# Optimization experiments

Hardware: AMD Instinct MI355X
Metric: run time of the kernel (lower is better)

## Reference

```python
import jax, jax.numpy as jnp
import numpy as np

N = 50000        # nodes
E = 600000       # edges (avg degree 12)
NODE, EDGE, GDIM = 15, 10, 8
HID, L, H = 128, 3, 4
D = HID // H     # per-head dim = 32


def setup_inputs() -> dict:
    key = jax.random.key(0)
    ks = jax.random.split(key, 32)
    f = lambda i, shape, s=0.05: jax.random.normal(ks[i], shape, dtype=jnp.float32) * s
    return {
        "x": f(0, (N, NODE), 1.0),
        "edge_index": jax.random.randint(ks[1], (2, E), 0, N, dtype=jnp.int32),
        "edge_attr": f(2, (E, EDGE), 1.0),
        "u": f(3, (GDIM,), 1.0),
        "enc_w": f(4, (NODE, HID)), "enc_b": f(5, (HID,)),
        "gat_lin_w": f(6, (L, HID, HID)),
        "gat_att_src": f(7, (L, H, D)), "gat_att_dst": f(8, (L, H, D)),
        "gat_lin_edge": f(9, (L, EDGE, HID)), "gat_att_edge": f(10, (L, H, D)),
        "gat_bias": f(11, (L, HID)),
        "ln_g": jnp.ones((L, HID), jnp.float32), "ln_b": jnp.zeros((L, HID), jnp.float32),
        "pool_w": f(12, (3 * HID + GDIM, GDIM)), "pool_b": f(13, (GDIM,)),
        "pool_ln_g": jnp.ones((GDIM,), jnp.float32), "pool_ln_b": jnp.zeros((GDIM,), jnp.float32),
        "head_w1": f(14, (4, HID, 32)), "head_b1": f(15, (4, 32)),
        "head_w2": f(16, (4, 32, 1)), "head_b2": f(17, (4, 1)),
        "strat_w1": f(18, (HID, 32)), "strat_b1": f(19, (32,)),
        "strat_w2": f(20, (32, 5)), "strat_b2": f(21, (5,)),
        "glob_w1": f(22, (GDIM, 32)), "glob_b1": f(23, (32,)),
        "glob_w2": f(24, (32, 4)), "glob_b2": f(25, (4,)),
    }


def _layer_norm(x, g, b, eps=1e-5):
    mu = jnp.mean(x, axis=-1, keepdims=True)
    var = jnp.mean(jnp.square(x - mu), axis=-1, keepdims=True)
    return (x - mu) * jax.lax.rsqrt(var + eps) * g + b


def _forward(edge_index, x, edge_attr, u, enc_w, enc_b, gat_lin_w, gat_att_src,
             gat_att_dst, gat_lin_edge, gat_att_edge, gat_bias, ln_g, ln_b,
             pool_w, pool_b, pool_ln_g, pool_ln_b, head_w1, head_b1, head_w2,
             head_b2, strat_w1, strat_b1, strat_w2, strat_b2, glob_w1, glob_b1,
             glob_w2, glob_b2):
    src0, dst0 = edge_index[0], edge_index[1]
    # PyG GATConv add_self_loops=True with fill_value='mean': self-loop edge
    # attr for node i = mean of edge_attr over edges whose dst is i.
    cnt = jax.ops.segment_sum(jnp.ones((E,), jnp.float32), dst0, num_segments=N)
    ea_self = jax.ops.segment_sum(edge_attr, dst0, num_segments=N) / jnp.maximum(cnt, 1.0)[:, None]
    loop = jnp.arange(N, dtype=src0.dtype)
    src = jnp.concatenate([src0, loop])
    dst = jnp.concatenate([dst0, loop])
    ea = jnp.concatenate([edge_attr, ea_self], axis=0)   # [E+N, EDGE]

    h = jax.nn.relu(x @ enc_w + enc_b)                   # node encoder [N, HID]
    for l in range(L):
        hp = (h @ gat_lin_w[l]).reshape(N, H, D)         # projected nodes
        a_s = jnp.sum(hp * gat_att_src[l], axis=-1)      # [N, H]
        a_d = jnp.sum(hp * gat_att_dst[l], axis=-1)
        ep = (ea @ gat_lin_edge[l]).reshape(-1, H, D)    # [E+N, H, D]
        a_e = jnp.sum(ep * gat_att_edge[l], axis=-1)     # [E+N, H]
        alpha = jax.nn.leaky_relu(a_s[src] + a_d[dst] + a_e, negative_slope=0.2)
        # numerically-stable softmax over incoming edges per dst node
        m = jax.ops.segment_max(alpha, dst, num_segments=N)
        w = jnp.exp(alpha - m[dst])
        denom = jax.ops.segment_sum(w, dst, num_segments=N)
        attn = w / denom[dst]                            # every node has a self-loop
        out = jax.ops.segment_sum(hp[src] * attn[..., None], dst, num_segments=N)
        out = out.reshape(N, HID) + gat_bias[l]
        # residual (shapes match) + dropout(eval=id) + layer norm
        h = _layer_norm(h + out, ln_g[l], ln_b[l])

    pooled = jnp.concatenate([h.mean(0), h.max(0), h.sum(0), u])[None]  # [1, 3*HID+GDIM]
    g = _layer_norm(jax.nn.relu(pooled @ pool_w + pool_b), pool_ln_g, pool_ln_b)

    # four stacked 128->32->1 heads (priority:tanh, coop/urgency/safety:sigmoid)
    z = jax.nn.relu(jnp.einsum('nf,kfh->knh', h, head_w1) + head_b1[:, None, :])
    y = jnp.einsum('knh,kho->kno', z, head_w2) + head_b2[:, None, :]   # [4, N, 1]
    priority = jnp.tanh(y[0])
    cooperation = jax.nn.sigmoid(y[1])
    urgency = jax.nn.sigmoid(y[2])
    safety = jax.nn.sigmoid(y[3])
    strategies = jax.nn.softmax(jax.nn.relu(h @ strat_w1 + strat_b1) @ strat_w2 + strat_b2, axis=-1)
    global_signal = jnp.tanh(jax.nn.relu(g @ glob_w1 + glob_b1) @ glob_w2 + glob_b2)[0]  # [4]
    return (priority, cooperation, urgency, safety, strategies, global_signal)


def reference(x, edge_index, edge_attr, u, enc_w, enc_b, gat_lin_w, gat_att_src,
              gat_att_dst, gat_lin_edge, gat_att_edge, gat_bias, ln_g, ln_b,
              pool_w, pool_b, pool_ln_g, pool_ln_b, head_w1, head_b1, head_w2,
              head_b2, strat_w1, strat_b1, strat_w2, strat_b2, glob_w1, glob_b1,
              glob_w2, glob_b2):
    return _forward(edge_index, x, edge_attr, u, enc_w, enc_b, gat_lin_w,
                    gat_att_src, gat_att_dst, gat_lin_edge, gat_att_edge,
                    gat_bias, ln_g, ln_b, pool_w, pool_b, pool_ln_g, pool_ln_b,
                    head_w1, head_b1, head_w2, head_b2, strat_w1, strat_b1,
                    strat_w2, strat_b2, glob_w1, glob_b1, glob_w2, glob_b2)
```

## Files before the change

### kernel.cpp

```cpp
#include <hip/hip_runtime.h>
#include <hip/hip_bf16.h>
#include <hip/hip_fp16.h>

#define N_NODES 50000
#define N_EDGES 600000
#define TOT_E   (N_EDGES + N_NODES)
#define NLAYER  3
#define PB      200
#define SCB     512
#define NSB     ((N_NODES + SCB - 1)/SCB)
#define CAP     96

typedef __hip_bfloat16 bf16;
typedef __attribute__((ext_vector_type(8))) short short8;
typedef __attribute__((ext_vector_type(4))) float floatx4;

__device__ __forceinline__ float b2f(bf16 v){ return __bfloat162float(v); }

__device__ __forceinline__ float ldm(const void* p, long i, int m){
  return m ? ((const float*)p)[i] : b2f(((const bf16*)p)[i]);
}

__device__ __forceinline__ unsigned bfr(float f){
  unsigned u = __float_as_uint(f);
  return (u + 0x7fffu + ((u>>16)&1u)) >> 16;
}

__global__ void detect_kernel(const void* probe, int* mode){
  __shared__ float red[256];
  int t = threadIdx.x;
  const bf16* p = (const bf16*)probe;
  float mx = 0.f;
  for (int i = t; i < 1920; i += 256){
    float v = fabsf(b2f(p[i]));
    if (!isfinite(v)) v = 1e30f;
    mx = fmaxf(mx, v);
  }
  red[t] = mx; __syncthreads();
  if (t == 0){
    float m = 0.f;
    for (int i = 0; i < 256; i++) m = fmaxf(m, red[i]);
    mode[0] = (m > 1000.0f) ? 1 : 0;
  }
}

__global__ void sentinel_kernel(int host_code, const int* devflags, const int* mode, float* out){
  if (threadIdx.x == 0 && blockIdx.x == 0){
    int code = host_code;
    if (!code && devflags){
      if (devflags[1] > 900)      code = 16384;
      else if (devflags[0])       code = 20480;
    }
    if (code){
      if (mode) code += 512*mode[0];
      out[0] = (float)code;
    }
  }
}

struct CvtTab { const void* s[27]; float* d[27]; int n[27]; };
__global__ void cvt_small_kernel(CvtTab tab, const int* mode){
  int b = blockIdx.x;
  int i = blockIdx.y*256 + threadIdx.x;
  if (i < tab.n[b]) tab.d[b][i] = ldm(tab.s[b], i, mode[0]);
}

__global__ void count_kernel(const int* __restrict__ ei, int* __restrict__ cnt, int* devflags){
  int e = blockIdx.x*256 + threadIdx.x;
  if (e >= N_EDGES) return;
  int s = ei[e], d = ei[N_EDGES + e];
  if (((unsigned)s >= N_NODES) || ((unsigned)d >= N_NODES)) atomicOr(&devflags[0], 1);
  else atomicAdd(&cnt[d], 1);
  if (e < 1024 && ei[2*e + 1] == 0) atomicAdd(&devflags[1], 1);
}

__global__ __launch_bounds__(SCB) void scan1_kernel(const int* __restrict__ cnt, int* __restrict__ bsum){
  __shared__ int ws[SCB/64];
  int i = blockIdx.x*SCB + threadIdx.x;
  int v = (i < N_NODES) ? cnt[i] + 1 : 0;
  int lane = threadIdx.x & 63, w = threadIdx.x >> 6;
  #pragma unroll
  for (int off = 1; off < 64; off <<= 1) v += __shfl_xor(v, off);
  if (lane == 0) ws[w] = v;
  __syncthreads();
  if (threadIdx.x == 0){
    int s = 0;
    #pragma unroll
    for (int k = 0; k < SCB/64; k++) s += ws[k];
    bsum[blockIdx.x] = s;
  }
}

__global__ void scan2_kernel(int* __restrict__ bsum, int* __restrict__ rowptr){
  if (threadIdx.x == 0 && blockIdx.x == 0){
    int run = 0;
    for (int b = 0; b < NSB; b++){ int t = bsum[b]; bsum[b] = run; run += t; }
    rowptr[N_NODES] = run;
  }
}

__global__ __launch_bounds__(SCB) void scan3_kernel(const int* __restrict__ cnt, const int* __restrict__ bsum,
                                                    int* __restrict__ rowptr){
  __shared__ int sm[SCB];
  int t = threadIdx.x;
  int i = blockIdx.x*SCB + t;
  int v = (i < N_NODES) ? cnt[i] + 1 : 0;
  sm[t] = v; __syncthreads();
  for (int off = 1; off < SCB; off <<= 1){
    int add = (t >= off) ? sm[t-off] : 0;
    __syncthreads();
    sm[t] += add;
    __syncthreads();
  }
  if (i < N_NODES) rowptr[i] = bsum[blockIdx.x] + sm[t] - v;
}

__global__ void scatter_kernel(const int* __restrict__ ei, const int* __restrict__ rowptr,
                               int* __restrict__ fill, int* __restrict__ srcs, int* __restrict__ pos_of){
  int e = blockIdx.x*256 + threadIdx.x;
  if (e >= TOT_E) return;
  if (e < N_EDGES){
    int s = ei[e], d = ei[N_EDGES + e];
    int pos = rowptr[d] + atomicAdd(&fill[d], 1);
    srcs[pos] = s; pos_of[e] = pos;
  } else {
    int i = e - N_EDGES;
    srcs[rowptr[i+1] - 1] = i;
  }
}

__global__ void pack_kernel(const float* __restrict__ head_w1, const float* __restrict__ strat_w1,
                            const float* __restrict__ head_b1, const float* __restrict__ strat_b1,
                            float* __restrict__ W1cat, float* __restrict__ b1cat){
  int t = blockIdx.x*256 + threadIdx.x;
  if (t < 128*160){
    int f = t / 160, c = t % 160;
    W1cat[t] = (c < 128) ? head_w1[(c>>5)*4096 + f*32 + (c&31)]
                         : strat_w1[f*32 + (c-128)];
  }
  if (t < 160) b1cat[t] = (t < 128) ? head_b1[t] : strat_b1[t-128];
}

__global__ void mmat_kernel(const float* __restrict__ We, const float* __restrict__ att_edge,
                            float* __restrict__ M){
  int t = threadIdx.x;
  if (t >= 120) return;
  int l = t / 40, r = t % 40, k = r / 4, hh = r % 4;
  float s = 0;
  #pragma unroll
  for (int d = 0; d < 32; d++)
    s += We[l*1280 + k*128 + hh*32 + d] * att_edge[l*128 + hh*32 + d];
  M[t] = s;
}

__global__ void vsd_kernel(const float* __restrict__ Wl, const float* __restrict__ att_src,
                           const float* __restrict__ att_dst, float* __restrict__ vsd){
  int t = blockIdx.x*256 + threadIdx.x;
  if (t >= 3*128*8) return;
  int l = t >> 10, r = t & 1023;
  int k = r >> 3, c = r & 7;
  int sd = c >> 2, hh = c & 3;
  const float* w = Wl + l*16384 + k*128 + hh*32;
  const float* a = (sd ? att_dst : att_src) + l*128 + hh*32;
  float s = 0;
  #pragma unroll
  for (int d = 0; d < 32; d++) s += w[d]*a[d];
  vsd[t] = s;
}

__global__ void pack_bsw_kernel(const float* __restrict__ Wl, const float* __restrict__ vsd,
                                const float* __restrict__ W1cat,
                                ushort* __restrict__ Bsw0, ushort* __restrict__ Bsw1){
  int tid = blockIdx.x*256 + threadIdx.x;
  if (tid < 3*4*144*32){
    int l = tid / 18432, rr = tid % 18432;
    int kt = rr / 4608, r2 = rr % 4608;
    int n = r2 / 32, kk = r2 & 31;
    int k = kt*32 + kk;
    float f;
    if (n < 128)      f = Wl[l*16384 + k*128 + n];
    else if (n < 136) f = vsd[l*1024 + k*8 + (n - 128)];
    else              f = 0.f;
    unsigned hb = bfr(f);
    float fh = __uint_as_float(hb<<16);
    unsigned lb = bfr(f - fh);
    Bsw0[(size_t)(l*2+0)*18432 + kt*4608 + n*32 + kk] = (ushort)hb;
    Bsw0[(size_t)(l*2+1)*18432 + kt*4608 + n*32 + kk] = (ushort)lb;
  } else {
    int t2 = tid - 3*4*144*32;
    if (t2 >= 4*160*32) return;
    int kt = t2 / 5120, r2 = t2 % 5120;
    int n = r2 / 32, kk = r2 & 31;
    int k = kt*32 + kk;
    float f = W1cat[k*160 + n];
    unsigned hb = bfr(f);
    float fh = __uint_as_float(hb<<16);
    unsigned lb = bfr(f - fh);
    Bsw1[kt*5120 + n*32 + kk]          = (ushort)hb;
    Bsw1[4*5120 + kt*5120 + n*32 + kk] = (ushort)lb;
  }
}

__global__ __launch_bounds__(128) void encoder_kernel(const void* __restrict__ x_raw, const int* __restrict__ mode,
                                                      const float* __restrict__ enc_w, const float* __restrict__ enc_b,
                                                      float* __restrict__ h){
  __shared__ float xs[16];
  int n = blockIdx.x, j = threadIdx.x;
  if (j < 15) xs[j] = ldm(x_raw, (long)n*15 + j, mode[0]);
  __syncthreads();
  float acc = enc_b[j];
  #pragma unroll
  for (int k = 0; k < 15; k++) acc += xs[k] * enc_w[k*128 + j];
  h[(size_t)n*128 + j] = fmaxf(acc, 0.0f);
}

__global__ void ae_kernel(const void* __restrict__ ea_raw, const int* __restrict__ mode,
                          const float* __restrict__ Mmat, const int* __restrict__ pos_of,
                          float4* __restrict__ aec){
  int e = blockIdx.x*256 + threadIdx.x;
  if (e >= N_EDGES) return;
  int m = mode[0];
  float v[10];
  #pragma unroll
  for (int k = 0; k < 10; k++) v[k] = ldm(ea_raw, (long)e*10 + k, m);
  int p = pos_of[e];
  #pragma unroll
  for (int l = 0; l < 3; l++){
    float r[4];
    #pragma unroll
    for (int hh = 0; hh < 4; hh++){
      float s = 0;
      #pragma unroll
      for (int k = 0; k < 10; k++) s += v[k]*Mmat[l*40 + k*4 + hh];
      r[hh] = s;
    }
    aec[(size_t)l*TOT_E + p] = make_float4(r[0], r[1], r[2], r[3]);
  }
}

template<int NT, int MODE>
__global__ __launch_bounds__(256) void gemm_mfma(
    const float* __restrict__ A, const ushort* __restrict__ Bhi, const ushort* __restrict__ Blo,
    int M, const float* __restrict__ bias, __half* __restrict__ Ch, float* __restrict__ Cf,
    float* __restrict__ a_s, float* __restrict__ a_d){
  int wv = threadIdx.x >> 6, lane = threadIdx.x & 63;
  int nl = lane & 15, q = lane >> 4;
  int row0 = blockIdx.x*64 + wv*16;
  if (row0 >= M) return;
  floatx4 acc[NT];
  #pragma unroll
  for (int t = 0; t < NT; t++) acc[t] = (floatx4){0.f, 0.f, 0.f, 0.f};
  int ra = row0 + nl; if (ra > M-1) ra = M-1;
  const float* arow = A + (size_t)ra*128 + q*8;
  #pragma unroll
  for (int kt = 0; kt < 4; kt++){
    float4 a0 = *(const float4*)(arow + kt*32);
    float4 a1 = *(const float4*)(arow + kt*32 + 4);
    float af[8] = {a0.x,a0.y,a0.z,a0.w,a1.x,a1.y,a1.z,a1.w};
    short8 ahi, alo;
    #pragma unroll
    for (int j = 0; j < 8; j++){
      unsigned hb = bfr(af[j]);
      float fh = __uint_as_float(hb<<16);
      unsigned lb = bfr(af[j] - fh);
      ahi[j] = (short)hb; alo[j] = (short)lb;
    }
    const ushort* bh = Bhi + kt*(NT*16*32) + nl*32 + q*8;
    const ushort* bl = Blo + kt*(NT*16*32) + nl*32 + q*8;
    #pragma unroll
    for (int t = 0; t < NT; t++){
      short8 b0 = *(const short8*)(bh + t*512);
      short8 b1 = *(const short8*)(bl + t*512);
      acc[t] = __builtin_amdgcn_mfma_f32_16x16x32_bf16(ahi, b0, acc[t], 0, 0, 0);
      acc[t] = __builtin_amdgcn_mfma_f32_16x16x32_bf16(alo, b0, acc[t], 0, 0, 0);
      acc[t] = __builtin_amdgcn_mfma_f32_16x16x32_bf16(ahi, b1, acc[t], 0, 0, 0);
    }
  }
  #pragma unroll
  for (int r = 0; r < 4; r++){
    int row = row0 + q*4 + r;
    if (row >= M) continue;
    if (MODE == 0){
      #pragma unroll
      for (int t = 0; t < 8; t++)
        Ch[(size_t)row*128 + t*16 + nl] = __float2half(acc[t][r]);
      if (nl < 4)      a_s[row*4 + nl]       = acc[8][r];
      else if (nl < 8) a_d[row*4 + (nl - 4)] = acc[8][r];
    } else {
      #pragma unroll
      for (int t = 0; t < NT; t++){
        int col = t*16 + nl;
        Cf[(size_t)row*160 + col] = fmaxf(acc[t][r] + bias[col], 0.f);
      }
    }
  }
}

__global__ __launch_bounds__(256) void fused_agg_kernel(
    const __half* __restrict__ hp, const float* __restrict__ a_s, const float* __restrict__ a_d,
    const float* __restrict__ aecl, const int* __restrict__ srcs, const int* __restrict__ rowptr,
    const float* __restrict__ bias_l, const float* __restrict__ ln_g_l,
    const float* __restrict__ ln_b_l, float* __restrict__ h){
  __shared__ float wsm[4][CAP*4];
  __shared__ int   ssm[4][CAP];
  int wv = threadIdx.x >> 6;
  int n = blockIdx.x*4 + wv;
  int lane = threadIdx.x & 63;
  int p0 = rowptr[n], p1 = rowptr[n+1];
  int deg = p1 - p0 - 1;
  int hh = lane & 3;
  int esl = lane >> 2;
  float adv = a_d[n*4 + hh];
  float asn = a_s[n*4 + hh];
  bool fits = (deg <= CAP);

  float m = -3.4e38f, ls = 0.f, ssum = 0.f;
  for (int base = 0; base < deg; base += 16){
    int idx = base + esl;
    if (idx < deg){
      int p = p0 + idx;
      float aev = aecl[(size_t)p*4 + hh];
      int sv = srcs[p];
      float al = a_s[sv*4 + hh] + adv + aev;
      al = (al > 0.f) ? al : 0.2f*al;
      ssum += aev;
      if (fits){
        wsm[wv][idx*4 + hh] = al;
        if (hh == 0) ssm[wv][idx] = sv;
      }
      if (al > m){ ls = ls*__expf(m - al) + 1.f; m = al; }
      else ls += __expf(al - m);
    }
  }
  #pragma unroll
  for (int off = 4; off <= 32; off <<= 1){
    float mo = __shfl_xor(m, off);
    float lo = __shfl_xor(ls, off);
    float so = __shfl_xor(ssum, off);
    ssum += so;
    float mn = fmaxf(m, mo);
    ls = ls*__expf(m - mn) + lo*__expf(mo - mn);
    m = mn;
  }
  float aself = ssum / (float)(deg > 0 ? deg : 1);
  float als = asn + adv + aself;
  als = (als > 0.f) ? als : 0.2f*als;
  float mx = fmaxf(m, als);
  float denom = ls*__expf(m - mx) + __expf(als - mx);
  float invd = 1.f/denom;

  if (fits){
    for (int base = 0; base < deg; base += 16){
      int idx = base + esl;
      if (idx < deg){
        float al = wsm[wv][idx*4 + hh];
        wsm[wv][idx*4 + hh] = __expf(al - mx)*invd;
      }
    }
  }

  int hsel = lane >> 4;
  float mxh   = __shfl(mx, hsel);
  float invdh = __shfl(invd, hsel);
  float alsh  = __shfl(als, hsel);

  float acc0 = 0.f, acc1 = 0.f;
  if (fits){
    for (int j = 0; j < deg; j++){
      float w = wsm[wv][j*4 + hsel];
      int  sj = ssm[wv][j];
      __half2 hv = *((const __half2*)(hp + (size_t)sj*128) + lane);
      acc0 += w*__half2float(hv.x);
      acc1 += w*__half2float(hv.y);
    }
  } else {
    for (int base = 0; base < deg; base += 16){
      int idx = base + esl;
      float wgt = 0.f; int sv = 0;
      if (idx < deg){
        int p = p0 + idx;
        float aev = aecl[(size_t)p*4 + hh];
        sv = srcs[p];
        float al = a_s[sv*4 + hh] + adv + aev;
        al = (al > 0.f) ? al : 0.2f*al;
        wgt = __expf(al - mx)*invd;
      }
      int cnt_e = min(16, deg - base);
      for (int j = 0; j < cnt_e; j++){
        float w = __shfl(wgt, j*4 + hsel);
        int  sj = __shfl(sv,  j*4);
        __half2 hv = *((const __half2*)(hp + (size_t)sj*128) + lane);
        acc0 += w*__half2float(hv.x);
        acc1 += w*__half2float(hv.y);
      }
    }
  }
  {
    float w = __expf(alsh - mxh)*invdh;
    __half2 hv = *((const __half2*)(hp + (size_t)n*128) + lane);
    acc0 += w*__half2float(hv.x);
    acc1 += w*__half2float(hv.y);
  }
  float2 res = *(const float2*)(h + (size_t)n*128 + lane*2);
  float2 bi  = *(const float2*)(bias_l + lane*2);
  float v0 = acc0 + bi.x + res.x;
  float v1 = acc1 + bi.y + res.y;
  float s = v0 + v1, sq = v0*v0 + v1*v1;
  #pragma unroll
  for (int off = 32; off >= 1; off >>= 1){ s += __shfl_xor(s, off); sq += __shfl_xor(sq, off); }
  float mu  = s * (1.0f/128.0f);
  float var = sq * (1.0f/128.0f) - mu*mu;
  float rs  = rsqrtf(fmaxf(var, 0.0f) + 1e-5f);
  float2 g  = *(const float2*)(ln_g_l + lane*2);
  float2 bb = *(const float2*)(ln_b_l + lane*2);
  float2 o;
  o.x = (v0 - mu)*rs*g.x + bb.x;
  o.y = (v1 - mu)*rs*g.y + bb.y;
  *(float2*)(h + (size_t)n*128 + lane*2) = o;
}

__global__ __launch_bounds__(128) void pool_part_kernel(const float* __restrict__ h,
                                                        float* __restrict__ psum, float* __restrict__ pmax){
  int b = blockIdx.x, j = threadIdx.x;
  int nb = b*(N_NODES/PB), ne = nb + (N_NODES/PB);
  float s = 0, m = -3.4e38f;
  for (int n = nb; n < ne; n++){ float v = h[(size_t)n*128 + j]; s += v; m = fmaxf(m, v); }
  psum[b*128 + j] = s; pmax[b*128 + j] = m;
}

__global__ __launch_bounds__(128) void global_kernel(
    const float* __restrict__ psum, const float* __restrict__ pmax,
    const float* __restrict__ u, const float* __restrict__ pool_w, const float* __restrict__ pool_b,
    const float* __restrict__ pool_ln_g, const float* __restrict__ pool_ln_b,
    const float* __restrict__ glob_w1, const float* __restrict__ glob_b1,
    const float* __restrict__ glob_w2, const float* __restrict__ glob_b2, float* __restrict__ out_glob){
  __shared__ float pooled[392];
  __shared__ float gv[8];
  __shared__ float t1[32];
  __shared__ float mv[2];
  int t = threadIdx.x;
  float s = 0, m = -3.4e38f;
  for (int b = 0; b < PB; b++){ s += psum[b*128 + t]; m = fmaxf(m, pmax[b*128 + t]); }
  pooled[t]       = s * (1.0f/(float)N_NODES);
  pooled[128 + t] = m;
  pooled[256 + t] = s;
  if (t < 8) pooled[384 + t] = u[t];
  __syncthreads();
  if (t < 8){
    float acc = pool_b[t];
    for (int f = 0; f < 392; f++) acc += pooled[f]*pool_w[f*8 + t];
    gv[t] = fmaxf(acc, 0.0f);
  }
  __syncthreads();
  if (t == 0){
    float mu = 0; for (int i = 0; i < 8; i++) mu += gv[i];
    mu *= 0.125f;
    float var = 0; for (int i = 0; i < 8; i++){ float d = gv[i]-mu; var += d*d; }
    var *= 0.125f;
    mv[0] = mu; mv[1] = rsqrtf(var + 1e-5f);
  }
  __syncthreads();
  float gnorm = (t < 8) ? (gv[t]-mv[0])*mv[1]*pool_ln_g[t] + pool_ln_b[t] : 0.0f;
  __syncthreads();
  if (t < 8) gv[t] = gnorm;
  __syncthreads();
  if (t < 32){
    float acc = glob_b1[t];
    for (int q = 0; q < 8; q++) acc += gv[q]*glob_w1[q*32 + t];
    t1[t] = fmaxf(acc, 0.0f);
  }
  __syncthreads();
  if (t < 4){
    float acc = glob_b2[t];
    for (int mm = 0; mm < 32; mm++) acc += t1[mm]*glob_w2[mm*4 + t];
    out_glob[t] = tanhf(acc);
  }
}

__global__ void finalize_kernel(
    const float* __restrict__ z, const float* __restrict__ head_w2, const float* __restrict__ head_b2,
    const float* __restrict__ strat_w2, const float* __restrict__ strat_b2, float* __restrict__ out){
  int n = blockIdx.x*256 + threadIdx.x;
  if (n >= N_NODES) return;
  const float* zr = z + (size_t)n*160;
  float y[4];
  #pragma unroll
  for (int k = 0; k < 4; k++){
    float acc = head_b2[k];
    #pragma unroll
    for (int m = 0; m < 32; m++) acc += zr[k*32+m]*head_w2[k*32+m];
    y[k] = acc;
  }
  out[n]             = tanhf(y[0]);
  out[N_NODES + n]   = 1.0f/(1.0f + expf(-y[1]));
  out[2*N_NODES + n] = 1.0f/(1.0f + expf(-y[2]));
  out[3*N_NODES + n] = 1.0f/(1.0f + expf(-y[3]));
  float sv[5], mx = -3.4e38f;
  #pragma unroll
  for (int j = 0; j < 5; j++){
    float acc = strat_b2[j];
    #pragma unroll
    for (int m = 0; m < 32; m++) acc += zr[128+m]*strat_w2[m*5+j];
    sv[j] = acc; mx = fmaxf(mx, acc);
  }
  float se = 0;
  #pragma unroll
  for (int j = 0; j < 5; j++){ sv[j] = expf(sv[j]-mx); se += sv[j]; }
  float inv = 1.0f/se;
  #pragma unroll
  for (int j = 0; j < 5; j++) out[4*N_NODES + (size_t)n*5 + j] = sv[j]*inv;
}

extern "C" void kernel_launch(void* const* d_in, const int* in_sizes, int n_in,
                              void* d_out, int out_size, void* d_ws, size_t ws_size,
                              hipStream_t stream){
  float* out = (float*)d_out;

  static const int exp_sizes[30] = {
    750000, 1200000, 6000000, 8, 1920, 128, 49152, 384, 384, 3840, 384,
    384, 384, 384, 3136, 8, 8, 8, 16384, 128, 128, 4, 4096, 32, 160, 5,
    256, 32, 128, 4 };
  int host_code = 0;
  if (n_in != 30){
    int nn = n_in < 0 ? 0 : (n_in > 63 ? 63 : n_in);
    host_code = 4096 + 32*nn;
  } else {
    for (int i = 0; i < 30; i++)
      if (in_sizes[i] != exp_sizes[i]){ host_code = 1024 + 8*i; break; }
  }
  if (!host_code && out_size != 9*N_NODES + 4) host_code = 12288;
  if (host_code){
    sentinel_kernel<<<1, 64, 0, stream>>>(host_code, nullptr, nullptr, out);
    return;
  }

  const int* ei = (const int*)d_in[1];

  char* wsp = (char*)d_ws;
  size_t off = 0;
  auto alloc = [&](size_t bytes)->char*{ char* p = wsp + off; off += (bytes + 255) & ~(size_t)255; return p; };

  float*  h    = (float*)alloc((size_t)N_NODES*128*4);
  __half* hp   = (__half*)alloc((size_t)N_NODES*128*2);
  float*  a_s  = (float*)alloc((size_t)N_NODES*4*4);
  float*  a_d  = (float*)alloc((size_t)N_NODES*4*4);
  float*  aec  = (float*)alloc((size_t)3*TOT_E*16);
  float*  zbuf = (float*)hp;
  int*   srcs   = (int*)alloc((size_t)TOT_E*4);
  int*   pos_of = (int*)alloc((size_t)N_EDGES*4);
  int*   rowptr = (int*)alloc((size_t)(N_NODES+1)*4);
  int*   bsum   = (int*)alloc((size_t)NSB*4);

  const int SN = 27;
  static const int sn_sizes[SN] = {
    8, 1920, 128, 49152, 384, 384, 3840, 384, 384, 384, 384,
    3136, 8, 8, 8, 16384, 128, 128, 4, 4096, 32, 160, 5, 256, 32, 128, 4 };
  static const int sn_input[SN] = {
    3, 4, 5, 6, 7, 8, 9, 10, 11, 12, 13, 14, 15, 16, 17,
    18, 19, 20, 21, 22, 23, 24, 25, 26, 27, 28, 29 };
  float* sarr[SN];
  for (int i = 0; i < SN; i++) sarr[i] = (float*)alloc((size_t)sn_sizes[i]*4);
  float* u_c       = sarr[0];
  float* enc_w_c   = sarr[1];
  float* enc_b_c   = sarr[2];
  float* Wl        = sarr[3];
  float* att_src_c = sarr[4];
  float* att_dst_c = sarr[5];
  float* lin_e_c   = sarr[6];
  float* att_e_c   = sarr[7];
  float* bias_c    = sarr[8];
  float* ln_g_c    = sarr[9];
  float* ln_b_c    = sarr[10];
  float* pool_w_c  = sarr[11];
  float* pool_b_c  = sarr[12];
  float* pln_g_c   = sarr[13];
  float* pln_b_c   = sarr[14];
  float* head_w1_c = sarr[15];
  float* head_b1_c = sarr[16];
  float* head_w2_c = sarr[17];
  float* head_b2_c = sarr[18];
  float* strat_w1_c= sarr[19];
  float* strat_b1_c= sarr[20];
  float* strat_w2_c= sarr[21];
  float* strat_b2_c= sarr[22];
  float* glob_w1_c = sarr[23];
  float* glob_b1_c = sarr[24];
  float* glob_w2_c = sarr[25];
  float* glob_b2_c = sarr[26];

  float*  W1cat = (float*)alloc((size_t)128*160*4);
  float*  b1cat = (float*)alloc(160*4);
  float*  Mmat  = (float*)alloc(3*40*4);
  float*  vsd   = (float*)alloc((size_t)3*128*8*4);
  ushort* Bsw0  = (ushort*)alloc((size_t)3*2*4*144*32*2);
  ushort* Bsw1  = (ushort*)alloc((size_t)2*4*160*32*2);
  int*    mode  = (int*)alloc(256);
  float*  psum  = (float*)alloc((size_t)PB*128*4);
  float*  pmax  = (float*)alloc((size_t)PB*128*4);
  size_t zero_begin = off;
  int*   devflags = (int*)alloc(256);
  int*   cnt      = (int*)alloc((size_t)N_NODES*4);
  int*   fill     = (int*)alloc((size_t)N_NODES*4);
  size_t zero_bytes = off - zero_begin;

  if (ws_size < off){
    sentinel_kernel<<<1, 64, 0, stream>>>(8192, nullptr, nullptr, out);
    return;
  }

  hipMemsetAsync(wsp + zero_begin, 0, zero_bytes, stream);

  detect_kernel<<<1, 256, 0, stream>>>(d_in[4], mode);

  CvtTab tab;
  for (int i = 0; i < SN; i++){ tab.s[i] = d_in[sn_input[i]]; tab.d[i] = sarr[i]; tab.n[i] = sn_sizes[i]; }
  cvt_small_kernel<<<dim3(SN, 192), 256, 0, stream>>>(tab, mode);

  pack_kernel<<<(128*160 + 255)/256, 256, 0, stream>>>(head_w1_c, strat_w1_c, head_b1_c, strat_b1_c, W1cat, b1cat);
  mmat_kernel<<<1, 128, 0, stream>>>(lin_e_c, att_e_c, Mmat);
  vsd_kernel<<<(3*128*8 + 255)/256, 256, 0, stream>>>(Wl, att_src_c, att_dst_c, vsd);
  pack_bsw_kernel<<<(3*4*144*32 + 4*160*32 + 255)/256, 256, 0, stream>>>(Wl, vsd, W1cat, Bsw0, Bsw1);

  count_kernel<<<(N_EDGES + 255)/256, 256, 0, stream>>>(ei, cnt, devflags);
  scan1_kernel<<<NSB, SCB, 0, stream>>>(cnt, bsum);
  scan2_kernel<<<1, 64, 0, stream>>>(bsum, rowptr);
  scan3_kernel<<<NSB, SCB, 0, stream>>>(cnt, bsum, rowptr);
  scatter_kernel<<<(TOT_E + 255)/256, 256, 0, stream>>>(ei, rowptr, fill, srcs, pos_of);
  ae_kernel<<<(N_EDGES + 255)/256, 256, 0, stream>>>(d_in[2], mode, Mmat, pos_of, (float4*)aec);
  encoder_kernel<<<N_NODES, 128, 0, stream>>>(d_in[0], mode, enc_w_c, enc_b_c, h);

  const int gb = (N_NODES + 63)/64;
  for (int l = 0; l < NLAYER; l++){
    const ushort* Bhi = Bsw0 + (size_t)l*2*18432;
    const ushort* Blo = Bhi + 18432;
    gemm_mfma<9,0><<<gb, 256, 0, stream>>>(h, Bhi, Blo, N_NODES, nullptr, hp, nullptr, a_s, a_d);
    fused_agg_kernel<<<N_NODES/4, 256, 0, stream>>>(hp, a_s, a_d, aec + (size_t)l*TOT_E*4, srcs, rowptr,
                                                    bias_c + l*128, ln_g_c + l*128, ln_b_c + l*128, h);
  }

  pool_part_kernel<<<PB, 128, 0, stream>>>(h, psum, pmax);
  global_kernel<<<1, 128, 0, stream>>>(psum, pmax, u_c, pool_w_c, pool_b_c, pln_g_c, pln_b_c,
                                       glob_w1_c, glob_b1_c, glob_w2_c, glob_b2_c, out + 9*N_NODES);
  gemm_mfma<10,1><<<gb, 256, 0, stream>>>(h, Bsw1, Bsw1 + 4*5120, N_NODES, b1cat, nullptr, zbuf,
                                          nullptr, nullptr);
  finalize_kernel<<<(N_NODES + 255)/256, 256, 0, stream>>>(zbuf, head_w2_c, head_b2_c, strat_w2_c, strat_b2_c, out);
  sentinel_kernel<<<1, 64, 0, stream>>>(0, devflags, mode, out);
}
```

Baseline: 531.0 us.

## Store node features as bf16 hi/lo split and fuse head finalize into GEMM

Node features are now stored as a pre-split bf16 hi/lo pair, written by the encoder and aggregation kernels, instead of fp32. The GEMMs therefore load ready-made MFMA operands and skip the per-element split. The head GEMM epilogue now applies bias, ReLU, the second-layer dot products via shuffle reductions, and the activations/softmax, which removes the z buffer round trip and the finalize kernel. Memory traffic for h stays the same size, and the hi+lo reconstruction keeps precision near fp32, with slight rounding differences possible.

```diff
diff --git a/kernel.cpp b/kernel.cpp
--- a/kernel.cpp
+++ b/kernel.cpp
@@ -24,6 +24,15 @@
 __device__ __forceinline__ unsigned bfr(float f){
   unsigned u = __float_as_uint(f);
   return (u + 0x7fffu + ((u>>16)&1u)) >> 16;
+}
+__device__ __forceinline__ void splitbf(float f, ushort& hi, ushort& lo){
+  unsigned hb = bfr(f);
+  float fh = __uint_as_float(hb<<16);
+  hi = (ushort)hb;
+  lo = (ushort)bfr(f - fh);
+}
+__device__ __forceinline__ float unpk(ushort hi, ushort lo){
+  return __uint_as_float((unsigned)hi<<16) + __uint_as_float((unsigned)lo<<16);
 }
 
 __global__ void detect_kernel(const void* probe, int* mode){
@@ -181,29 +190,24 @@
     if (n < 128)      f = Wl[l*16384 + k*128 + n];
     else if (n < 136) f = vsd[l*1024 + k*8 + (n - 128)];
     else              f = 0.f;
-    unsigned hb = bfr(f);
-    float fh = __uint_as_float(hb<<16);
-    unsigned lb = bfr(f - fh);
-    Bsw0[(size_t)(l*2+0)*18432 + kt*4608 + n*32 + kk] = (ushort)hb;
-    Bsw0[(size_t)(l*2+1)*18432 + kt*4608 + n*32 + kk] = (ushort)lb;
+    ushort hb, lb; splitbf(f, hb, lb);
+    Bsw0[(size_t)(l*2+0)*18432 + kt*4608 + n*32 + kk] = hb;
+    Bsw0[(size_t)(l*2+1)*18432 + kt*4608 + n*32 + kk] = lb;
   } else {
     int t2 = tid - 3*4*144*32;
     if (t2 >= 4*160*32) return;
     int kt = t2 / 5120, r2 = t2 % 5120;
     int n = r2 / 32, kk = r2 & 31;
     int k = kt*32 + kk;
-    float f = W1cat[k*160 + n];
-    unsigned hb = bfr(f);
-    float fh = __uint_as_float(hb<<16);
-    unsigned lb = bfr(f - fh);
-    Bsw1[kt*5120 + n*32 + kk]          = (ushort)hb;
-    Bsw1[4*5120 + kt*5120 + n*32 + kk] = (ushort)lb;
+    ushort hb, lb; splitbf(W1cat[k*160 + n], hb, lb);
+    Bsw1[kt*5120 + n*32 + kk]          = hb;
+    Bsw1[4*5120 + kt*5120 + n*32 + kk] = lb;
   }
 }
 
 __global__ __launch_bounds__(128) void encoder_kernel(const void* __restrict__ x_raw, const int* __restrict__ mode,
                                                       const float* __restrict__ enc_w, const float* __restrict__ enc_b,
-                                                      float* __restrict__ h){
+                                                      ushort* __restrict__ h_hi, ushort* __restrict__ h_lo){
   __shared__ float xs[16];
   int n = blockIdx.x, j = threadIdx.x;
   if (j < 15) xs[j] = ldm(x_raw, (long)n*15 + j, mode[0]);
@@ -211,7 +215,10 @@
   float acc = enc_b[j];
   #pragma unroll
   for (int k = 0; k < 15; k++) acc += xs[k] * enc_w[k*128 + j];
-  h[(size_t)n*128 + j] = fmaxf(acc, 0.0f);
+  acc = fmaxf(acc, 0.0f);
+  ushort hi, lo; splitbf(acc, hi, lo);
+  h_hi[(size_t)n*128 + j] = hi;
+  h_lo[(size_t)n*128 + j] = lo;
 }
 
 __global__ void ae_kernel(const void* __restrict__ ea_raw, const int* __restrict__ mode,
@@ -240,9 +247,12 @@
 
 template<int NT, int MODE>
 __global__ __launch_bounds__(256) void gemm_mfma(
-    const float* __restrict__ A, const ushort* __restrict__ Bhi, const ushort* __restrict__ Blo,
-    int M, const float* __restrict__ bias, __half* __restrict__ Ch, float* __restrict__ Cf,
-    float* __restrict__ a_s, float* __restrict__ a_d){
+    const ushort* __restrict__ Ahi, const ushort* __restrict__ Alo,
+    const ushort* __restrict__ Bhi, const ushort* __restrict__ Blo,
+    int M, const float* __restrict__ bias, __half* __restrict__ Ch,
+    float* __restrict__ a_s, float* __restrict__ a_d,
+    const float* __restrict__ hw2, const float* __restrict__ hb2,
+    const float* __restrict__ sw2, const float* __restrict__ sb2, float* __restrict__ out){
   int wv = threadIdx.x >> 6, lane = threadIdx.x & 63;
   int nl = lane & 15, q = lane >> 4;
   int row0 = blockIdx.x*64 + wv*16;
@@ -251,20 +261,12 @@
   #pragma unroll
   for (int t = 0; t < NT; t++) acc[t] = (floatx4){0.f, 0.f, 0.f, 0.f};
   int ra = row0 + nl; if (ra > M-1) ra = M-1;
-  const float* arow = A + (size_t)ra*128 + q*8;
+  const ushort* ah = Ahi + (size_t)ra*128 + q*8;
+  const ushort* al = Alo + (size_t)ra*128 + q*8;
   #pragma unroll
   for (int kt = 0; kt < 4; kt++){
-    float4 a0 = *(const float4*)(arow + kt*32);
-    float4 a1 = *(const float4*)(arow + kt*32 + 4);
-    float af[8] = {a0.x,a0.y,a0.z,a0.w,a1.x,a1.y,a1.z,a1.w};
-    short8 ahi, alo;
-    #pragma unroll
-    for (int j = 0; j < 8; j++){
-      unsigned hb = bfr(af[j]);
-      float fh = __uint_as_float(hb<<16);
-      unsigned lb = bfr(af[j] - fh);
-      ahi[j] = (short)hb; alo[j] = (short)lb;
-    }
+    short8 ahi = *(const short8*)(ah + kt*32);
+    short8 alo = *(const short8*)(al + kt*32);
     const ushort* bh = Bhi + kt*(NT*16*32) + nl*32 + q*8;
     const ushort* bl = Blo + kt*(NT*16*32) + nl*32 + q*8;
     #pragma unroll
@@ -276,21 +278,68 @@
       acc[t] = __builtin_amdgcn_mfma_f32_16x16x32_bf16(ahi, b1, acc[t], 0, 0, 0);
     }
   }
-  #pragma unroll
-  for (int r = 0; r < 4; r++){
-    int row = row0 + q*4 + r;
-    if (row >= M) continue;
-    if (MODE == 0){
+  if (MODE == 0){
+    #pragma unroll
+    for (int r = 0; r < 4; r++){
+      int row = row0 + q*4 + r;
+      if (row >= M) continue;
       #pragma unroll
       for (int t = 0; t < 8; t++)
         Ch[(size_t)row*128 + t*16 + nl] = __float2half(acc[t][r]);
       if (nl < 4)      a_s[row*4 + nl]       = acc[8][r];
       else if (nl < 8) a_d[row*4 + (nl - 4)] = acc[8][r];
-    } else {
+    }
+  } else {
+    float b1v[NT], hw2v[8], sw2v[10];
+    #pragma unroll
+    for (int t = 0; t < NT; t++) b1v[t] = bias[t*16 + nl];
+    #pragma unroll
+    for (int t = 0; t < 8; t++) hw2v[t] = hw2[t*16 + nl];
+    #pragma unroll
+    for (int t = 0; t < 2; t++)
       #pragma unroll
-      for (int t = 0; t < NT; t++){
-        int col = t*16 + nl;
-        Cf[(size_t)row*160 + col] = fmaxf(acc[t][r] + bias[col], 0.f);
+      for (int j = 0; j < 5; j++) sw2v[t*5 + j] = sw2[(t*16 + nl)*5 + j];
+    #pragma unroll
+    for (int r = 0; r < 4; r++){
+      int row = row0 + q*4 + r;
+      float pk[4] = {0,0,0,0};
+      float sv[5] = {0,0,0,0,0};
+      #pragma unroll
+      for (int t = 0; t < 8; t++){
+        float z = fmaxf(acc[t][r] + b1v[t], 0.f);
+        pk[t>>1] += z*hw2v[t];
+      }
+      #pragma unroll
+      for (int t = 0; t < 2; t++){
+        float z = fmaxf(acc[8+t][r] + b1v[8+t], 0.f);
+        #pragma unroll
+        for (int j = 0; j < 5; j++) sv[j] += z*sw2v[t*5 + j];
+      }
+      #pragma unroll
+      for (int off = 1; off <= 8; off <<= 1){
+        #pragma unroll
+        for (int k = 0; k < 4; k++) pk[k] += __shfl_xor(pk[k], off);
+        #pragma unroll
+        for (int j = 0; j < 5; j++) sv[j] += __shfl_xor(sv[j], off);
+      }
+      if (nl == 0 && row < M){
+        float y0 = pk[0] + hb2[0];
+        float y1 = pk[1] + hb2[1];
+        float y2 = pk[2] + hb2[2];
+        float y3 = pk[3] + hb2[3];
+        out[row]             = tanhf(y0);
+        out[N_NODES + row]   = 1.f/(1.f + __expf(-y1));
+        out[2*N_NODES + row] = 1.f/(1.f + __expf(-y2));
+        out[3*N_NODES + row] = 1.f/(1.f + __expf(-y3));
+        float s5[5], mxs = -3.4e38f;
+        #pragma unroll
+        for (int j = 0; j < 5; j++){ s5[j] = sv[j] + sb2[j]; mxs = fmaxf(mxs, s5[j]); }
+        float se = 0;
+        #pragma unroll
+        for (int j = 0; j < 5; j++){ s5[j] = __expf(s5[j] - mxs); se += s5[j]; }
+        float inv = 1.f/se;
+        #pragma unroll
+        for (int j = 0; j < 5; j++) out[4*N_NODES + (size_t)row*5 + j] = s5[j]*inv;
       }
     }
   }
@@ -300,7 +349,7 @@
     const __half* __restrict__ hp, const float* __restrict__ a_s, const float* __restrict__ a_d,
     const float* __restrict__ aecl, const int* __restrict__ srcs, const int* __restrict__ rowptr,
     const float* __restrict__ bias_l, const float* __restrict__ ln_g_l,
-    const float* __restrict__ ln_b_l, float* __restrict__ h){
+    const float* __restrict__ ln_b_l, ushort* __restrict__ h_hi, ushort* __restrict__ h_lo){
   __shared__ float wsm[4][CAP*4];
   __shared__ int   ssm[4][CAP];
   int wv = threadIdx.x >> 6;
@@ -401,10 +450,11 @@
     acc0 += w*__half2float(hv.x);
     acc1 += w*__half2float(hv.y);
   }
-  float2 res = *(const float2*)(h + (size_t)n*128 + lane*2);
+  ushort2 rh = *(const ushort2*)(h_hi + (size_t)n*128 + lane*2);
+  ushort2 rl = *(const ushort2*)(h_lo + (size_t)n*128 + lane*2);
   float2 bi  = *(const float2*)(bias_l + lane*2);
-  float v0 = acc0 + bi.x + res.x;
-  float v1 = acc1 + bi.y + res.y;
+  float v0 = acc0 + bi.x + unpk(rh.x, rl.x);
+  float v1 = acc1 + bi.y + unpk(rh.y, rl.y);
   float s = v0 + v1, sq = v0*v0 + v1*v1;
   #pragma unroll
   for (int off = 32; off >= 1; off >>= 1){ s += __shfl_xor(s, off); sq += __shfl_xor(sq, off); }
@@ -413,18 +463,25 @@
   float rs  = rsqrtf(fmaxf(var, 0.0f) + 1e-5f);
   float2 g  = *(const float2*)(ln_g_l + lane*2);
   float2 bb = *(const float2*)(ln_b_l + lane*2);
-  float2 o;
-  o.x = (v0 - mu)*rs*g.x + bb.x;
-  o.y = (v1 - mu)*rs*g.y + bb.y;
-  *(float2*)(h + (size_t)n*128 + lane*2) = o;
-}
-
-__global__ __launch_bounds__(128) void pool_part_kernel(const float* __restrict__ h,
+  float o0 = (v0 - mu)*rs*g.x + bb.x;
+  float o1 = (v1 - mu)*rs*g.y + bb.y;
+  ushort2 oh, ol;
+  splitbf(o0, oh.x, ol.x);
+  splitbf(o1, oh.y, ol.y);
+  *(ushort2*)(h_hi + (size_t)n*128 + lane*2) = oh;
+  *(ushort2*)(h_lo + (size_t)n*128 + lane*2) = ol;
+}
+
+__global__ __launch_bounds__(128) void pool_part_kernel(const ushort* __restrict__ h_hi,
+                                                        const ushort* __restrict__ h_lo,
                                                         float* __restrict__ psum, float* __restrict__ pmax){
   int b = blockIdx.x, j = threadIdx.x;
   int nb = b*(N_NODES/PB), ne = nb + (N_NODES/PB);
   float s = 0, m = -3.4e38f;
-  for (int n = nb; n < ne; n++){ float v = h[(size_t)n*128 + j]; s += v; m = fmaxf(m, v); }
+  for (int n = nb; n < ne; n++){
+    float v = unpk(h_hi[(size_t)n*128 + j], h_lo[(size_t)n*128 + j]);
+    s += v; m = fmaxf(m, v);
+  }
   psum[b*128 + j] = s; pmax[b*128 + j] = m;
 }
 
@@ -477,40 +534,6 @@
   }
 }
 
-__global__ void finalize_kernel(
-    const float* __restrict__ z, const float* __restrict__ head_w2, const float* __restrict__ head_b2,
-    const float* __restrict__ strat_w2, const float* __restrict__ strat_b2, float* __restrict__ out){
-  int n = blockIdx.x*256 + threadIdx.x;
-  if (n >= N_NODES) return;
-  const float* zr = z + (size_t)n*160;
-  float y[4];
-  #pragma unroll
-  for (int k = 0; k < 4; k++){
-    float acc = head_b2[k];
-    #pragma unroll
-    for (int m = 0; m < 32; m++) acc += zr[k*32+m]*head_w2[k*32+m];
-    y[k] = acc;
-  }
-  out[n]             = tanhf(y[0]);
-  out[N_NODES + n]   = 1.0f/(1.0f + expf(-y[1]));
-  out[2*N_NODES + n] = 1.0f/(1.0f + expf(-y[2]));
-  out[3*N_NODES + n] = 1.0f/(1.0f + expf(-y[3]));
-  float sv[5], mx = -3.4e38f;
-  #pragma unroll
-  for (int j = 0; j < 5; j++){
-    float acc = strat_b2[j];
-    #pragma unroll
-    for (int m = 0; m < 32; m++) acc += zr[128+m]*strat_w2[m*5+j];
-    sv[j] = acc; mx = fmaxf(mx, acc);
-  }
-  float se = 0;
-  #pragma unroll
-  for (int j = 0; j < 5; j++){ sv[j] = expf(sv[j]-mx); se += sv[j]; }
-  float inv = 1.0f/se;
-  #pragma unroll
-  for (int j = 0; j < 5; j++) out[4*N_NODES + (size_t)n*5 + j] = sv[j]*inv;
-}
-
 extern "C" void kernel_launch(void* const* d_in, const int* in_sizes, int n_in,
                               void* d_out, int out_size, void* d_ws, size_t ws_size,
                               hipStream_t stream){
@@ -540,12 +563,12 @@
   size_t off = 0;
   auto alloc = [&](size_t bytes)->char*{ char* p = wsp + off; off += (bytes + 255) & ~(size_t)255; return p; };
 
-  float*  h    = (float*)alloc((size_t)N_NODES*128*4);
+  ushort* h_hi = (ushort*)alloc((size_t)N_NODES*128*2);
+  ushort* h_lo = (ushort*)alloc((size_t)N_NODES*128*2);
   __half* hp   = (__half*)alloc((size_t)N_NODES*128*2);
   float*  a_s  = (float*)alloc((size_t)N_NODES*4*4);
   float*  a_d  = (float*)alloc((size_t)N_NODES*4*4);
   float*  aec  = (float*)alloc((size_t)3*TOT_E*16);
-  float*  zbuf = (float*)hp;
   int*   srcs   = (int*)alloc((size_t)TOT_E*4);
   int*   pos_of = (int*)alloc((size_t)N_EDGES*4);
   int*   rowptr = (int*)alloc((size_t)(N_NODES+1)*4);
@@ -627,22 +650,22 @@
   scan3_kernel<<<NSB, SCB, 0, stream>>>(cnt, bsum, rowptr);
   scatter_kernel<<<(TOT_E + 255)/256, 256, 0, stream>>>(ei, rowptr, fill, srcs, pos_of);
   ae_kernel<<<(N_EDGES + 255)/256, 256, 0, stream>>>(d_in[2], mode, Mmat, pos_of, (float4*)aec);
-  encoder_kernel<<<N_NODES, 128, 0, stream>>>(d_in[0], mode, enc_w_c, enc_b_c, h);
+  encoder_kernel<<<N_NODES, 128, 0, stream>>>(d_in[0], mode, enc_w_c, enc_b_c, h_hi, h_lo);
 
   const int gb = (N_NODES + 63)/64;
   for (int l = 0; l < NLAYER; l++){
     const ushort* Bhi = Bsw0 + (size_t)l*2*18432;
     const ushort* Blo = Bhi + 18432;
-    gemm_mfma<9,0><<<gb, 256, 0, stream>>>(h, Bhi, Blo, N_NODES, nullptr, hp, nullptr, a_s, a_d);
+    gemm_mfma<9,0><<<gb, 256, 0, stream>>>(h_hi, h_lo, Bhi, Blo, N_NODES, nullptr, hp, a_s, a_d,
+                                           nullptr, nullptr, nullptr, nullptr, nullptr);
     fused_agg_kernel<<<N_NODES/4, 256, 0, stream>>>(hp, a_s, a_d, aec + (size_t)l*TOT_E*4, srcs, rowptr,
-                                                    bias_c + l*128, ln_g_c + l*128, ln_b_c + l*128, h);
-  }
-
-  pool_part_kernel<<<PB, 128, 0, stream>>>(h, psum, pmax);
+                                                    bias_c + l*128, ln_g_c + l*128, ln_b_c + l*128, h_hi, h_lo);
+  }
+
+  pool_part_kernel<<<PB, 128, 0, stream>>>(h_hi, h_lo, psum, pmax);
   global_kernel<<<1, 128, 0, stream>>>(psum, pmax, u_c, pool_w_c, pool_b_c, pln_g_c, pln_b_c,
                                        glob_w1_c, glob_b1_c, glob_w2_c, glob_b2_c, out + 9*N_NODES);
-  gemm_mfma<10,1><<<gb, 256, 0, stream>>>(h, Bsw1, Bsw1 + 4*5120, N_NODES, b1cat, nullptr, zbuf,
-                                          nullptr, nullptr);
-  finalize_kernel<<<(N_NODES + 255)/256, 256, 0, stream>>>(zbuf, head_w2_c, head_b2_c, strat_w2_c, strat_b2_c, out);
+  gemm_mfma<10,1><<<gb, 256, 0, stream>>>(h_hi, h_lo, Bsw1, Bsw1 + 4*5120, N_NODES, b1cat, nullptr,
+                                          nullptr, nullptr, head_w2_c, head_b2_c, strat_w2_c, strat_b2_c, out);
   sentinel_kernel<<<1, 64, 0, stream>>>(0, devflags, mode, out);
 }
```

Result: no change. 537.9 us (+1.3%).
